# Kernel tuning notes

Hardware: AMD Instinct MI355X
Metric: run time of the kernel (lower is better)

The kernel has to match this reference:

```python
import jax, jax.numpy as jnp
import numpy as np

B, C, H, W = 2, 256, 32, 32
D_MODEL = C
D_INNER = 2 * D_MODEL          # 512
D_STATE = 16
DT_RANK = (D_MODEL + 15) // 16  # 16
D_CONV = 4
LN_EPS = 1e-5


def setup_inputs() -> dict:
    key = jax.random.key(0)
    ks = jax.random.split(key, 32)

    def nrm(k, shape, s=0.02):
        return (jax.random.normal(k, shape) * s).astype(jnp.float32)

    inp = {"x": jax.random.normal(ks[0], (B, C, H, W), dtype=jnp.float32)}
    # LayerNorm params
    inp["ln1_w"] = jnp.ones((D_MODEL,), jnp.float32)
    inp["ln1_b"] = jnp.zeros((D_MODEL,), jnp.float32)
    inp["ln2_w"] = jnp.ones((D_MODEL,), jnp.float32)
    inp["ln2_b"] = jnp.zeros((D_MODEL,), jnp.float32)
    # Two MambaBlocks with identical structure
    for i, p in enumerate(["m1", "m2"]):
        o = 1 + i * 11
        inp[p + "_in_w"] = nrm(ks[o + 0], (D_MODEL, 2 * D_INNER))
        inp[p + "_in_b"] = jnp.zeros((2 * D_INNER,), jnp.float32)
        inp[p + "_conv_w"] = nrm(ks[o + 1], (D_INNER, 1, D_CONV), 0.1)
        inp[p + "_conv_b"] = jnp.zeros((D_INNER,), jnp.float32)
        inp[p + "_xproj_w"] = nrm(ks[o + 2], (D_INNER, DT_RANK + 2 * D_STATE))
        inp[p + "_dt_w"] = nrm(ks[o + 3], (DT_RANK, D_INNER), 0.1)
        inp[p + "_dt_b"] = (jax.random.uniform(ks[o + 4], (D_INNER,)) * 0.1 - 4.0).astype(jnp.float32)
        # S4D-real init: A[d, n] = n+1
        inp[p + "_A_log"] = jnp.log(jnp.broadcast_to(jnp.arange(1, D_STATE + 1, dtype=jnp.float32), (D_INNER, D_STATE)))
        inp[p + "_D"] = jnp.ones((D_INNER,), jnp.float32)
        inp[p + "_out_w"] = nrm(ks[o + 5], (D_INNER, D_MODEL))
        inp[p + "_out_b"] = jnp.zeros((D_MODEL,), jnp.float32)
    return inp


def layernorm(x, w, b):
    mu = jnp.mean(x, axis=-1, keepdims=True)
    var = jnp.mean(jnp.square(x - mu), axis=-1, keepdims=True)
    return (x - mu) * jax.lax.rsqrt(var + LN_EPS) * w + b


def mamba_block(x, in_w, in_b, conv_w, conv_b, xproj_w, dt_w, dt_b, A_log, Dp, out_w, out_b):
    # x: (b, h, w, c) -> flatten spatial dims into the scan sequence
    b, h, w, c = x.shape
    L = h * w
    u = x.reshape(b, L, c)
    xr = u @ in_w + in_b                       # (b, L, 2*d_inner)
    xs, res = jnp.split(xr, 2, axis=-1)
    # depthwise causal conv1d over L
    xc = jnp.transpose(xs, (0, 2, 1))          # (b, d_inner, L)
    xc = jax.lax.conv_general_dilated(
        xc, conv_w, (1,), [(D_CONV - 1, 0)],
        dimension_numbers=("NCH", "OIH", "NCH"),
        feature_group_count=D_INNER) + conv_b[None, :, None]
    xs = jax.nn.silu(jnp.transpose(xc, (0, 2, 1)))  # (b, L, d_inner)
    # input-dependent SSM params
    x_dbl = xs @ xproj_w                       # (b, L, dt_rank + 2*n)
    dt, Bm, Cm = jnp.split(x_dbl, [DT_RANK, DT_RANK + D_STATE], axis=-1)
    delta = jax.nn.softplus(dt @ dt_w + dt_b)  # (b, L, d_inner)
    A = -jnp.exp(A_log)                        # (d_inner, n)
    dA = jnp.exp(delta[..., None] * A)                         # (b, L, d, n)
    dBu = delta[..., None] * Bm[:, :, None, :] * xs[..., None]  # (b, L, d, n)

    def step(hst, ins):
        dA_t, dBu_t, C_t = ins
        hst = dA_t * hst + dBu_t               # (b, d, n)
        y_t = jnp.einsum("bdn,bn->bd", hst, C_t)
        return hst, y_t

    h0 = jnp.zeros((b, D_INNER, D_STATE), dtype=xs.dtype)
    _, ys = jax.lax.scan(step, h0,
                         (jnp.swapaxes(dA, 0, 1), jnp.swapaxes(dBu, 0, 1), jnp.swapaxes(Cm, 0, 1)))
    y = jnp.swapaxes(ys, 0, 1) + xs * Dp       # (b, L, d_inner)
    y = y * jax.nn.silu(res)
    out = y @ out_w + out_b                    # (b, L, c)
    return out.reshape(b, h, w, c)


def reference(x, ln1_w, ln1_b, ln2_w, ln2_b,
              m1_in_w, m1_in_b, m1_conv_w, m1_conv_b, m1_xproj_w, m1_dt_w, m1_dt_b, m1_A_log, m1_D, m1_out_w, m1_out_b,
              m2_in_w, m2_in_b, m2_conv_w, m2_conv_b, m2_xproj_w, m2_dt_w, m2_dt_b, m2_A_log, m2_D, m2_out_w, m2_out_b):
    xt = jnp.transpose(x, (0, 2, 3, 1))  # b c h w -> b h w c
    xt = xt + layernorm(mamba_block(xt, m1_in_w, m1_in_b, m1_conv_w, m1_conv_b, m1_xproj_w,
                                    m1_dt_w, m1_dt_b, m1_A_log, m1_D, m1_out_w, m1_out_b), ln1_w, ln1_b)
    xt = jnp.flip(xt, axis=3)  # flip channel axis, as in the original
    xt = xt + layernorm(mamba_block(xt, m2_in_w, m2_in_b, m2_conv_w, m2_conv_b, m2_xproj_w,
                                    m2_dt_w, m2_dt_b, m2_A_log, m2_D, m2_out_w, m2_out_b), ln2_w, ln2_b)
    xt = jnp.flip(xt, axis=3)
    return jnp.transpose(xt, (0, 3, 1, 2))  # b h w c -> b c h w
```

## Files before the change

kernel.cpp:

```cpp
#include <hip/hip_runtime.h>
#include <hip/hip_bf16.h>
#include <math.h>

#define L 1024
#define NB 2
#define DM 256
#define DI 512
#define DS 16
#define DR 16
#define NC 64
#define CL 16

typedef unsigned int u32;
typedef short s16x8 __attribute__((ext_vector_type(8)));
typedef float f32x4 __attribute__((ext_vector_type(4)));

__device__ __forceinline__ float sigmoidf_(float x){ return 1.f/(1.f+__expf(-x)); }

__device__ __forceinline__ unsigned short f2bf(float v){
  u32 x = __float_as_uint(v);
  u32 r = (x + 0x7fffu + ((x >> 16) & 1u)) >> 16;
  return (unsigned short)r;
}

__device__ __forceinline__ void gload_lds16(const void* g, void* l){
  __builtin_amdgcn_global_load_lds((const __attribute__((address_space(1))) u32*)g,
                                   (__attribute__((address_space(3))) u32*)l, 16, 0, 0);
}

__device__ __forceinline__ void wave_reduce2(float& a, float& b){
  #pragma unroll
  for (int m=32; m; m>>=1){ a += __shfl_xor(a, m, 64); b += __shfl_xor(b, m, 64); }
}

#define SEG1 262144
#define SEG2 294912
#define SEG3 131072
#define SEGP (SEG1+SEG2+SEG3)
__global__ __launch_bounds__(256) void k_prep(
    const float* __restrict__ inw1, const float* __restrict__ xpw1, const float* __restrict__ dtw1, const float* __restrict__ outw1,
    const float* __restrict__ inw2, const float* __restrict__ xpw2, const float* __restrict__ dtw2, const float* __restrict__ outw2,
    unsigned short* __restrict__ Wt1i, unsigned short* __restrict__ Wt1x, unsigned short* __restrict__ Wt1o,
    unsigned short* __restrict__ Wt2i, unsigned short* __restrict__ Wt2x, unsigned short* __restrict__ Wt2o){
  int g = blockIdx.x*256 + threadIdx.x;
  int p = g >= SEGP;
  int r = g - p*SEGP;
  const float* inw = p ? inw2 : inw1;  const float* xpw = p ? xpw2 : xpw1;
  const float* dtw = p ? dtw2 : dtw1;  const float* outw = p ? outw2 : outw1;
  unsigned short* Wti = p ? Wt2i : Wt1i; unsigned short* Wtx = p ? Wt2x : Wt1x;
  unsigned short* Wto = p ? Wt2o : Wt1o;
  if (r < SEG1){
    int n = r >> 8, k = r & 255;
    Wti[r] = f2bf(inw[(size_t)k*1024 + n]);
  } else if (r < SEG1+SEG2){
    int q = r - SEG1; int n = q >> 9, k = q & 511;
    float v;
    if (n < 512){
      float acc = 0.f;
      #pragma unroll
      for (int j=0;j<16;++j) acc = fmaf(xpw[k*48 + j], dtw[j*512 + n], acc);
      v = acc;
    } else if (n < 544){
      v = xpw[k*48 + 16 + (n - 512)];
    } else v = 0.f;
    Wtx[q] = f2bf(v);
  } else {
    int q = r - SEG1 - SEG2; int n = q >> 9, k = q & 511;
    Wto[q] = f2bf(outw[(size_t)k*256 + n]);
  }
}

__global__ __launch_bounds__(256) void k_transpose_in(const float* __restrict__ x,
    float* __restrict__ u, unsigned short* __restrict__ ub){
  __shared__ float T[64][65];
  int t = threadIdx.x;
  int bidx = blockIdx.x;
  int lt = bidx & 15, ct = (bidx >> 4) & 3, b = bidx >> 6;
  int l0 = lt*64, c0 = ct*64;
  int lsub = (t & 15)*4, csub = t >> 4;
  #pragma unroll
  for (int i=0;i<4;++i){
    int c = csub + i*16;
    float4 v = *(const float4*)(x + ((size_t)(b*256 + c0 + c))*1024 + l0 + lsub);
    T[lsub+0][c]=v.x; T[lsub+1][c]=v.y; T[lsub+2][c]=v.z; T[lsub+3][c]=v.w;
  }
  __syncthreads();
  int cw = (t & 15)*4, lw = t >> 4;
  #pragma unroll
  for (int i=0;i<4;++i){
    int l = lw + i*16;
    float4 v = make_float4(T[l][cw], T[l][cw+1], T[l][cw+2], T[l][cw+3]);
    size_t o = ((size_t)(b*1024 + l0 + l))*256 + c0 + cw;
    *(float4*)(u + o) = v;
    *(ushort4*)(ub + o) = make_ushort4(f2bf(v.x), f2bf(v.y), f2bf(v.z), f2bf(v.w));
  }
}

__global__ __launch_bounds__(256) void k_gemm_mfma(const unsigned short* __restrict__ A,
    const unsigned short* __restrict__ Wt, const float* __restrict__ bias,
    float* __restrict__ C, int M, int N, int K){
  __shared__ __align__(16) unsigned short As[64*64];
  __shared__ __align__(16) unsigned short Bs[64*64];
  int tid = threadIdx.x;
  int lane = tid & 63;
  int wid  = tid >> 6;
  int bm = blockIdx.y * 64, bn = blockIdx.x * 64;
  int wm = (wid >> 1) * 32, wn = (wid & 1) * 32;
  int lrow = lane & 15, lg = lane >> 4;
  int srow = tid >> 3;
  int ssl  = tid & 7;
  int sswz = ssl ^ (srow & 7);

  f32x4 acc[2][2] = {};

  for (int k0 = 0; k0 < K; k0 += 64){
    #pragma unroll
    for (int i = 0; i < 2; ++i){
      int row = srow + i*32;
      gload_lds16(A  + (size_t)(bm + row)*K + k0 + sswz*8, &As[row*64 + ssl*8]);
      gload_lds16(Wt + (size_t)(bn + row)*K + k0 + sswz*8, &Bs[row*64 + ssl*8]);
    }
    __syncthreads();
    #pragma unroll
    for (int ks = 0; ks < 2; ++ks){
      int kg = ks*4 + lg;
      int swz = (kg ^ (lrow & 7)) << 3;
      s16x8 a[2], b[2];
      #pragma unroll
      for (int f = 0; f < 2; ++f){
        a[f] = *(const s16x8*)&As[(wm + f*16 + lrow)*64 + swz];
        b[f] = *(const s16x8*)&Bs[(wn + f*16 + lrow)*64 + swz];
      }
      #pragma unroll
      for (int i = 0; i < 2; ++i)
        #pragma unroll
        for (int j = 0; j < 2; ++j)
          acc[i][j] = __builtin_amdgcn_mfma_f32_16x16x32_bf16(a[i], b[j], acc[i][j], 0, 0, 0);
    }
    __syncthreads();
  }
  #pragma unroll
  for (int j = 0; j < 2; ++j){
    int col = bn + wn + j*16 + lrow;
    if (col < N){
      float bv = bias ? bias[col] : 0.f;
      #pragma unroll
      for (int i = 0; i < 2; ++i){
        #pragma unroll
        for (int r = 0; r < 4; ++r){
          int row = bm + wm + i*16 + lg*4 + r;
          C[(size_t)row*N + col] = acc[i][j][r] + bv;
        }
      }
    }
  }
}

__global__ __launch_bounds__(256) void k_gemm_xproj(const unsigned short* __restrict__ A,
    const unsigned short* __restrict__ Wt, const float* __restrict__ dtb,
    float* __restrict__ dlt, float* __restrict__ BC, int M){
  const int K = 512;
  __shared__ __align__(16) unsigned short As[64*64];
  __shared__ __align__(16) unsigned short Bs[64*64];
  int tid = threadIdx.x;
  int lane = tid & 63;
  int wid  = tid >> 6;
  int bm = blockIdx.y * 64, bn = blockIdx.x * 64;
  int wm = (wid >> 1) * 32, wn = (wid & 1) * 32;
  int lrow = lane & 15, lg = lane >> 4;
  int srow = tid >> 3;
  int ssl  = tid & 7;
  int sswz = ssl ^ (srow & 7);

  f32x4 acc[2][2] = {};

  for (int k0 = 0; k0 < K; k0 += 64){
    #pragma unroll
    for (int i = 0; i < 2; ++i){
      int row = srow + i*32;
      gload_lds16(A  + (size_t)(bm + row)*K + k0 + sswz*8, &As[row*64 + ssl*8]);
      gload_lds16(Wt + (size_t)(bn + row)*K + k0 + sswz*8, &Bs[row*64 + ssl*8]);
    }
    __syncthreads();
    #pragma unroll
    for (int ks = 0; ks < 2; ++ks){
      int kg = ks*4 + lg;
      int swz = (kg ^ (lrow & 7)) << 3;
      s16x8 a[2], b[2];
      #pragma unroll
      for (int f = 0; f < 2; ++f){
        a[f] = *(const s16x8*)&As[(wm + f*16 + lrow)*64 + swz];
        b[f] = *(const s16x8*)&Bs[(wn + f*16 + lrow)*64 + swz];
      }
      #pragma unroll
      for (int i = 0; i < 2; ++i)
        #pragma unroll
        for (int j = 0; j < 2; ++j)
          acc[i][j] = __builtin_amdgcn_mfma_f32_16x16x32_bf16(a[i], b[j], acc[i][j], 0, 0, 0);
    }
    __syncthreads();
  }
  #pragma unroll
  for (int j = 0; j < 2; ++j){
    int col = bn + wn + j*16 + lrow;
    if (col < 512){
      float bv = dtb[col];
      #pragma unroll
      for (int i = 0; i < 2; ++i){
        #pragma unroll
        for (int r = 0; r < 4; ++r){
          int row = bm + wm + i*16 + lg*4 + r;
          float a = acc[i][j][r] + bv;
          dlt[(size_t)row*512 + col] = fmaxf(a, 0.f) + log1pf(__expf(-fabsf(a)));
        }
      }
    } else if (col < 544){
      #pragma unroll
      for (int i = 0; i < 2; ++i){
        #pragma unroll
        for (int r = 0; r < 4; ++r){
          int row = bm + wm + i*16 + lg*4 + r;
          BC[(size_t)row*32 + (col - 512)] = acc[i][j][r];
        }
      }
    }
  }
}

__global__ __launch_bounds__(256) void k_conv_silu(const float* __restrict__ xr, const float* __restrict__ cw,
    const float* __restrict__ cb, float* __restrict__ xsc, unsigned short* __restrict__ xscb){
  int g = blockIdx.x*256 + threadIdx.x;
  int d = g & 511; int l = (g >> 9) & 1023; int b = g >> 19;
  float acc = cb[d];
  const float* w = cw + d*4;
  #pragma unroll
  for (int k=0;k<4;++k){
    int j = l + k - 3;
    if (j >= 0) acc = fmaf(w[k], xr[((size_t)(b*L + j))*(2*DI) + d], acc);
  }
  float v = acc * sigmoidf_(acc);
  xsc[g] = v; xscb[g] = f2bf(v);
}

__global__ __launch_bounds__(256) void k_scan_partial(const float* __restrict__ delta, const float* __restrict__ xsc,
    const float* __restrict__ BC, const float* __restrict__ A_log,
    float* __restrict__ hend, float* __restrict__ Ssum){
  int g = blockIdx.x*256 + threadIdx.x;
  int d = g & 511; int bc = g >> 9;
  int c = bc & (NC-1); int b = bc >> 6;
  float A[DS];
  #pragma unroll
  for (int n=0;n<DS;++n) A[n] = -__expf(A_log[d*DS + n]);
  float h[DS];
  #pragma unroll
  for (int n=0;n<DS;++n) h[n] = 0.f;
  float S = 0.f;
  int l0 = c*CL;
  for (int t=0;t<CL;++t){
    size_t ix = (size_t)(b*L + l0 + t);
    float dlt = delta[ix*DI + d];
    float xv  = xsc[ix*DI + d];
    S += dlt;
    float dx = dlt * xv;
    const float* bp = BC + ix*32;
    #pragma unroll
    for (int n=0;n<DS;++n){
      float dA = __expf(dlt * A[n]);
      h[n] = fmaf(dA, h[n], dx * bp[n]);
    }
  }
  #pragma unroll
  for (int n=0;n<DS;++n) hend[((size_t)bc*DS + n)*DI + d] = h[n];
  Ssum[(size_t)bc*DI + d] = S;
}

__global__ __launch_bounds__(256) void k_scan_combine(const float* __restrict__ hend, const float* __restrict__ Ssum,
    const float* __restrict__ A_log, float* __restrict__ hinit){
  int g = blockIdx.x*256 + threadIdx.x;
  int d = g & 511; int n = (g >> 9) & 15; int b = g >> 13;
  float A = -__expf(A_log[d*DS + n]);
  float h = 0.f;
  for (int c=0;c<NC;++c){
    int bc = b*NC + c;
    hinit[((size_t)bc*DS + n)*DI + d] = h;
    float dec = __expf(A * Ssum[(size_t)bc*DI + d]);
    h = fmaf(dec, h, hend[((size_t)bc*DS + n)*DI + d]);
  }
}

__global__ __launch_bounds__(256) void k_scan_final(const float* __restrict__ delta, const float* __restrict__ xsc,
    const float* __restrict__ BC, const float* __restrict__ xr, const float* __restrict__ A_log,
    const float* __restrict__ Dp, const float* __restrict__ hinit, unsigned short* __restrict__ ygb){
  int g = blockIdx.x*256 + threadIdx.x;
  int d = g & 511; int bc = g >> 9;
  int c = bc & (NC-1); int b = bc >> 6;
  float A[DS];
  #pragma unroll
  for (int n=0;n<DS;++n) A[n] = -__expf(A_log[d*DS + n]);
  float h[DS];
  #pragma unroll
  for (int n=0;n<DS;++n) h[n] = hinit[((size_t)bc*DS + n)*DI + d];
  float Dv = Dp[d];
  int l0 = c*CL;
  for (int t=0;t<CL;++t){
    size_t ix = (size_t)(b*L + l0 + t);
    float dlt = delta[ix*DI + d];
    float xv  = xsc[ix*DI + d];
    float res = xr[ix*(2*DI) + DI + d];
    float dx = dlt * xv;
    const float* bp = BC + ix*32;
    const float* cp = bp + 16;
    float y = 0.f;
    #pragma unroll
    for (int n=0;n<DS;++n){
      float dA = __expf(dlt * A[n]);
      h[n] = fmaf(dA, h[n], dx * bp[n]);
      y = fmaf(h[n], cp[n], y);
    }
    y = fmaf(xv, Dv, y);
    ygb[ix*DI + d] = f2bf(y * (res * sigmoidf_(res)));
  }
}

__global__ __launch_bounds__(256) void k_ln_flip(const float* __restrict__ mo, const float* __restrict__ resid,
    const float* __restrict__ w, const float* __restrict__ bias,
    float* __restrict__ u2, unsigned short* __restrict__ u2b){
  int row = blockIdx.x*4 + (threadIdx.x >> 6);
  int lane = threadIdx.x & 63;
  int c4 = lane*4;
  float4 xv = *(const float4*)(mo + (size_t)row*256 + c4);
  float s1 = xv.x+xv.y+xv.z+xv.w;
  float s2 = xv.x*xv.x+xv.y*xv.y+xv.z*xv.z+xv.w*xv.w;
  wave_reduce2(s1, s2);
  float mu = s1*(1.f/256), var = s2*(1.f/256) - mu*mu;
  float inv = rsqrtf(var + 1e-5f);
  float4 rv = *(const float4*)(resid + (size_t)row*256 + c4);
  float4 wv = *(const float4*)(w + c4);
  float4 bv = *(const float4*)(bias + c4);
  float o0 = rv.x + (xv.x-mu)*inv*wv.x + bv.x;
  float o1 = rv.y + (xv.y-mu)*inv*wv.y + bv.y;
  float o2 = rv.z + (xv.z-mu)*inv*wv.z + bv.z;
  float o3 = rv.w + (xv.w-mu)*inv*wv.w + bv.w;
  size_t o = (size_t)row*256 + (252 - c4);
  *(float4*)(u2 + o) = make_float4(o3, o2, o1, o0);
  *(ushort4*)(u2b + o) = make_ushort4(f2bf(o3), f2bf(o2), f2bf(o1), f2bf(o0));
}

__global__ __launch_bounds__(256) void k_ln_out(const float* __restrict__ mo, const float* __restrict__ resid,
    const float* __restrict__ w, const float* __restrict__ bias, float* __restrict__ out){
  int row = blockIdx.x*4 + (threadIdx.x >> 6);
  int lane = threadIdx.x & 63;
  int c4 = lane*4;
  int b = row >> 10, l = row & 1023;
  float4 xv = *(const float4*)(mo + (size_t)row*256 + c4);
  float s1 = xv.x+xv.y+xv.z+xv.w;
  float s2 = xv.x*xv.x+xv.y*xv.y+xv.z*xv.z+xv.w*xv.w;
  wave_reduce2(s1, s2);
  float mu = s1*(1.f/256), var = s2*(1.f/256) - mu*mu;
  float inv = rsqrtf(var + 1e-5f);
  float4 rv = *(const float4*)(resid + (size_t)row*256 + c4);
  float4 wv = *(const float4*)(w + c4);
  float4 bv = *(const float4*)(bias + c4);
  float o0 = rv.x + (xv.x-mu)*inv*wv.x + bv.x;
  float o1 = rv.y + (xv.y-mu)*inv*wv.y + bv.y;
  float o2 = rv.z + (xv.z-mu)*inv*wv.z + bv.z;
  float o3 = rv.w + (xv.w-mu)*inv*wv.w + bv.w;
  size_t base = ((size_t)b*256 + 255) << 10;
  out[base - ((size_t)(c4+0) << 10) + l] = o0;
  out[base - ((size_t)(c4+1) << 10) + l] = o1;
  out[base - ((size_t)(c4+2) << 10) + l] = o2;
  out[base - ((size_t)(c4+3) << 10) + l] = o3;
}

static void run_block(const unsigned short* ub, const float* inb, const float* cw, const float* cb,
                      const float* dtb, const float* Alog, const float* Dp, const float* ob,
                      const unsigned short* Wti, const unsigned short* Wtx, const unsigned short* Wto,
                      float* xr, float* xsc, unsigned short* xscb, float* dlt, float* BC,
                      unsigned short* ygb, float* hend, float* hinit, float* Ssum, float* mo,
                      hipStream_t stream){
  dim3 b256(256);
  k_gemm_mfma<<<dim3(16,32), b256, 0, stream>>>(ub, Wti, inb, xr, NB*L, 2*DI, DM);
  k_conv_silu<<<4096, b256, 0, stream>>>(xr, cw, cb, xsc, xscb);
  k_gemm_xproj<<<dim3(9,32), b256, 0, stream>>>(xscb, Wtx, dtb, dlt, BC, NB*L);
  k_scan_partial<<<NB*NC*DI/256, b256, 0, stream>>>(dlt, xsc, BC, Alog, hend, Ssum);
  k_scan_combine<<<NB*DS*DI/256, b256, 0, stream>>>(hend, Ssum, Alog, hinit);
  k_scan_final<<<NB*NC*DI/256, b256, 0, stream>>>(dlt, xsc, BC, xr, Alog, Dp, hinit, ygb);
  k_gemm_mfma<<<dim3(4,32), b256, 0, stream>>>(ygb, Wto, ob, mo, NB*L, DM, DI);
}

extern "C" void kernel_launch(void* const* d_in, const int* in_sizes, int n_in,
                              void* d_out, int out_size, void* d_ws, size_t ws_size,
                              hipStream_t stream) {
  const float* x    = (const float*)d_in[0];
  const float* ln1w = (const float*)d_in[1];
  const float* ln1b = (const float*)d_in[2];
  const float* ln2w = (const float*)d_in[3];
  const float* ln2b = (const float*)d_in[4];

  const float* m1[11]; const float* m2[11];
  for (int i=0;i<11;++i){ m1[i] = (const float*)d_in[5+i]; m2[i] = (const float*)d_in[16+i]; }

  float* ws = (float*)d_ws;
  float*          u0   = ws;
  unsigned short* u0b  = (unsigned short*)(ws + 524288);
  float*          xr   = ws + 655360;
  float*          xsc  = ws + 2752512;
  unsigned short* xscb = (unsigned short*)(ws + 3801088);
  float*          dlt  = ws + 4063232;
  float*          BC   = ws + 5111808;
  unsigned short* ygb  = (unsigned short*)(ws + 5177344);
  float*          hend = ws + 5439488;
  float*          hinit= ws + 6488064;
  float*          Ssum = ws + 7536640;
  float*          u2   = ws + 7602176;
  unsigned short* Wt1i = (unsigned short*)(ws + 8126464);
  unsigned short* Wt1x = (unsigned short*)(ws + 8257536);
  unsigned short* Wt1o = (unsigned short*)(ws + 8404992);
  unsigned short* Wt2i = (unsigned short*)(ws + 8470528);
  unsigned short* Wt2x = (unsigned short*)(ws + 8601600);
  unsigned short* Wt2o = (unsigned short*)(ws + 8749056);
  unsigned short* u2b = u0b;
  float* mo = hend;

  dim3 b256(256);
  k_prep<<<2*SEGP/256, b256, 0, stream>>>(m1[0], m1[4], m1[5], m1[9],
                                          m2[0], m2[4], m2[5], m2[9],
                                          Wt1i, Wt1x, Wt1o, Wt2i, Wt2x, Wt2o);
  k_transpose_in<<<128, b256, 0, stream>>>(x, u0, u0b);

  run_block(u0b, m1[1], m1[2], m1[3], m1[6], m1[7], m1[8], m1[10],
            Wt1i, Wt1x, Wt1o, xr, xsc, xscb, dlt, BC, ygb, hend, hinit, Ssum, mo, stream);
  k_ln_flip<<<512, b256, 0, stream>>>(mo, u0, ln1w, ln1b, u2, u2b);

  run_block(u2b, m2[1], m2[2], m2[3], m2[6], m2[7], m2[8], m2[10],
            Wt2i, Wt2x, Wt2o, xr, xsc, xscb, dlt, BC, ygb, hend, hinit, Ssum, mo, stream);
  k_ln_out<<<512, b256, 0, stream>>>(mo, u2, ln2w, ln2b, (float*)d_out);
}
```

Baseline: 155.6 us.

## Fuse scan stages, out-proj GEMM with LayerNorm, and prep with transpose

Merges the three scan kernels into one block-local kernel that keeps chunk end-states in LDS, which removes the hend/hinit global round trips and two launches. Fuses the output projection GEMM with the residual LayerNorm and flip, using a full-row 64x256 tile so row statistics can be reduced in-block. Also merges the weight prep with the input transpose, and vectorises the conv+silu to four channels per thread. The cost is less parallelism: the scan now runs only 256 blocks, the combine step is serial over 64 chunks on one wave, and the out-LN GEMM launches just 32 blocks.

```diff
diff --git a/kernel.cpp b/kernel.cpp
--- a/kernel.cpp
+++ b/kernel.cpp
@@ -28,21 +28,42 @@
                                    (__attribute__((address_space(3))) u32*)l, 16, 0, 0);
 }
 
-__device__ __forceinline__ void wave_reduce2(float& a, float& b){
-  #pragma unroll
-  for (int m=32; m; m>>=1){ a += __shfl_xor(a, m, 64); b += __shfl_xor(b, m, 64); }
-}
-
 #define SEG1 262144
 #define SEG2 294912
 #define SEG3 131072
 #define SEGP (SEG1+SEG2+SEG3)
-__global__ __launch_bounds__(256) void k_prep(
+__global__ __launch_bounds__(256) void k_prep_trans(const float* __restrict__ x,
+    float* __restrict__ u, unsigned short* __restrict__ ub,
     const float* __restrict__ inw1, const float* __restrict__ xpw1, const float* __restrict__ dtw1, const float* __restrict__ outw1,
     const float* __restrict__ inw2, const float* __restrict__ xpw2, const float* __restrict__ dtw2, const float* __restrict__ outw2,
     unsigned short* __restrict__ Wt1i, unsigned short* __restrict__ Wt1x, unsigned short* __restrict__ Wt1o,
     unsigned short* __restrict__ Wt2i, unsigned short* __restrict__ Wt2x, unsigned short* __restrict__ Wt2o){
-  int g = blockIdx.x*256 + threadIdx.x;
+  __shared__ float T[64][65];
+  if (blockIdx.x < 128){
+    int t = threadIdx.x;
+    int bidx = blockIdx.x;
+    int lt = bidx & 15, ct = (bidx >> 4) & 3, b = bidx >> 6;
+    int l0 = lt*64, c0 = ct*64;
+    int lsub = (t & 15)*4, csub = t >> 4;
+    #pragma unroll
+    for (int i=0;i<4;++i){
+      int c = csub + i*16;
+      float4 v = *(const float4*)(x + ((size_t)(b*256 + c0 + c))*1024 + l0 + lsub);
+      T[lsub+0][c]=v.x; T[lsub+1][c]=v.y; T[lsub+2][c]=v.z; T[lsub+3][c]=v.w;
+    }
+    __syncthreads();
+    int cw = (t & 15)*4, lw = t >> 4;
+    #pragma unroll
+    for (int i=0;i<4;++i){
+      int l = lw + i*16;
+      float4 v = make_float4(T[l][cw], T[l][cw+1], T[l][cw+2], T[l][cw+3]);
+      size_t o = ((size_t)(b*1024 + l0 + l))*256 + c0 + cw;
+      *(float4*)(u + o) = v;
+      *(ushort4*)(ub + o) = make_ushort4(f2bf(v.x), f2bf(v.y), f2bf(v.z), f2bf(v.w));
+    }
+    return;
+  }
+  int g = (blockIdx.x - 128)*256 + threadIdx.x;
   int p = g >= SEGP;
   int r = g - p*SEGP;
   const float* inw = p ? inw2 : inw1;  const float* xpw = p ? xpw2 : xpw1;
@@ -67,32 +88,6 @@
   } else {
     int q = r - SEG1 - SEG2; int n = q >> 9, k = q & 511;
     Wto[q] = f2bf(outw[(size_t)k*256 + n]);
-  }
-}
-
-__global__ __launch_bounds__(256) void k_transpose_in(const float* __restrict__ x,
-    float* __restrict__ u, unsigned short* __restrict__ ub){
-  __shared__ float T[64][65];
-  int t = threadIdx.x;
-  int bidx = blockIdx.x;
-  int lt = bidx & 15, ct = (bidx >> 4) & 3, b = bidx >> 6;
-  int l0 = lt*64, c0 = ct*64;
-  int lsub = (t & 15)*4, csub = t >> 4;
-  #pragma unroll
-  for (int i=0;i<4;++i){
-    int c = csub + i*16;
-    float4 v = *(const float4*)(x + ((size_t)(b*256 + c0 + c))*1024 + l0 + lsub);
-    T[lsub+0][c]=v.x; T[lsub+1][c]=v.y; T[lsub+2][c]=v.z; T[lsub+3][c]=v.w;
-  }
-  __syncthreads();
-  int cw = (t & 15)*4, lw = t >> 4;
-  #pragma unroll
-  for (int i=0;i<4;++i){
-    int l = lw + i*16;
-    float4 v = make_float4(T[l][cw], T[l][cw+1], T[l][cw+2], T[l][cw+3]);
-    size_t o = ((size_t)(b*1024 + l0 + l))*256 + c0 + cw;
-    *(float4*)(u + o) = v;
-    *(ushort4*)(ub + o) = make_ushort4(f2bf(v.x), f2bf(v.y), f2bf(v.z), f2bf(v.w));
   }
 }
 
@@ -227,27 +222,44 @@
   }
 }
 
-__global__ __launch_bounds__(256) void k_conv_silu(const float* __restrict__ xr, const float* __restrict__ cw,
+__global__ __launch_bounds__(256) void k_conv4(const float* __restrict__ xr, const float* __restrict__ cw,
     const float* __restrict__ cb, float* __restrict__ xsc, unsigned short* __restrict__ xscb){
   int g = blockIdx.x*256 + threadIdx.x;
-  int d = g & 511; int l = (g >> 9) & 1023; int b = g >> 19;
-  float acc = cb[d];
-  const float* w = cw + d*4;
+  int i4 = g << 2;
+  int d = i4 & 511; int l = (i4 >> 9) & 1023; int b = i4 >> 19;
+  float4 w0 = *(const float4*)(cw + (d+0)*4);
+  float4 w1 = *(const float4*)(cw + (d+1)*4);
+  float4 w2 = *(const float4*)(cw + (d+2)*4);
+  float4 w3 = *(const float4*)(cw + (d+3)*4);
+  float4 a = *(const float4*)(cb + d);
+  const float* p0 = (const float*)&w0; const float* p1 = (const float*)&w1;
+  const float* p2 = (const float*)&w2; const float* p3 = (const float*)&w3;
   #pragma unroll
   for (int k=0;k<4;++k){
     int j = l + k - 3;
-    if (j >= 0) acc = fmaf(w[k], xr[((size_t)(b*L + j))*(2*DI) + d], acc);
-  }
-  float v = acc * sigmoidf_(acc);
-  xsc[g] = v; xscb[g] = f2bf(v);
-}
-
-__global__ __launch_bounds__(256) void k_scan_partial(const float* __restrict__ delta, const float* __restrict__ xsc,
-    const float* __restrict__ BC, const float* __restrict__ A_log,
-    float* __restrict__ hend, float* __restrict__ Ssum){
-  int g = blockIdx.x*256 + threadIdx.x;
-  int d = g & 511; int bc = g >> 9;
-  int c = bc & (NC-1); int b = bc >> 6;
+    if (j >= 0){
+      float4 xv = *(const float4*)(xr + ((size_t)(b*L + j))*(2*DI) + d);
+      a.x = fmaf(p0[k], xv.x, a.x);
+      a.y = fmaf(p1[k], xv.y, a.y);
+      a.z = fmaf(p2[k], xv.z, a.z);
+      a.w = fmaf(p3[k], xv.w, a.w);
+    }
+  }
+  a.x *= sigmoidf_(a.x); a.y *= sigmoidf_(a.y);
+  a.z *= sigmoidf_(a.z); a.w *= sigmoidf_(a.w);
+  *(float4*)(xsc + i4) = a;
+  *(ushort4*)(xscb + i4) = make_ushort4(f2bf(a.x), f2bf(a.y), f2bf(a.z), f2bf(a.w));
+}
+
+__global__ __launch_bounds__(256) void k_scan_fused(const float* __restrict__ delta,
+    const float* __restrict__ xsc, const float* __restrict__ BC, const float* __restrict__ xr,
+    const float* __restrict__ A_log, const float* __restrict__ Dp, unsigned short* __restrict__ ygb){
+  __shared__ float hbuf[64][68];
+  __shared__ float SsumL[64][4];
+  int tid = threadIdx.x;
+  int chunk = tid >> 2, dl = tid & 3;
+  int b = blockIdx.x >> 7, d0 = (blockIdx.x & 127) << 2;
+  int d = d0 + dl;
   float A[DS];
   #pragma unroll
   for (int n=0;n<DS;++n) A[n] = -__expf(A_log[d*DS + n]);
@@ -255,7 +267,7 @@
   #pragma unroll
   for (int n=0;n<DS;++n) h[n] = 0.f;
   float S = 0.f;
-  int l0 = c*CL;
+  int l0 = chunk*CL;
   for (int t=0;t<CL;++t){
     size_t ix = (size_t)(b*L + l0 + t);
     float dlt = delta[ix*DI + d];
@@ -264,44 +276,28 @@
     float dx = dlt * xv;
     const float* bp = BC + ix*32;
     #pragma unroll
-    for (int n=0;n<DS;++n){
-      float dA = __expf(dlt * A[n]);
-      h[n] = fmaf(dA, h[n], dx * bp[n]);
-    }
-  }
-  #pragma unroll
-  for (int n=0;n<DS;++n) hend[((size_t)bc*DS + n)*DI + d] = h[n];
-  Ssum[(size_t)bc*DI + d] = S;
-}
-
-__global__ __launch_bounds__(256) void k_scan_combine(const float* __restrict__ hend, const float* __restrict__ Ssum,
-    const float* __restrict__ A_log, float* __restrict__ hinit){
-  int g = blockIdx.x*256 + threadIdx.x;
-  int d = g & 511; int n = (g >> 9) & 15; int b = g >> 13;
-  float A = -__expf(A_log[d*DS + n]);
-  float h = 0.f;
-  for (int c=0;c<NC;++c){
-    int bc = b*NC + c;
-    hinit[((size_t)bc*DS + n)*DI + d] = h;
-    float dec = __expf(A * Ssum[(size_t)bc*DI + d]);
-    h = fmaf(dec, h, hend[((size_t)bc*DS + n)*DI + d]);
-  }
-}
-
-__global__ __launch_bounds__(256) void k_scan_final(const float* __restrict__ delta, const float* __restrict__ xsc,
-    const float* __restrict__ BC, const float* __restrict__ xr, const float* __restrict__ A_log,
-    const float* __restrict__ Dp, const float* __restrict__ hinit, unsigned short* __restrict__ ygb){
-  int g = blockIdx.x*256 + threadIdx.x;
-  int d = g & 511; int bc = g >> 9;
-  int c = bc & (NC-1); int b = bc >> 6;
-  float A[DS];
-  #pragma unroll
-  for (int n=0;n<DS;++n) A[n] = -__expf(A_log[d*DS + n]);
-  float h[DS];
-  #pragma unroll
-  for (int n=0;n<DS;++n) h[n] = hinit[((size_t)bc*DS + n)*DI + d];
+    for (int n=0;n<DS;++n) h[n] = fmaf(__expf(dlt*A[n]), h[n], dx * bp[n]);
+  }
+  #pragma unroll
+  for (int n=0;n<DS;++n) hbuf[chunk][dl*16+n] = h[n];
+  SsumL[chunk][dl] = S;
+  __syncthreads();
+  if (tid < 64){
+    int dl2 = tid & 3, n2 = tid >> 2;
+    float An = -__expf(A_log[(d0+dl2)*DS + n2]);
+    float hh = 0.f;
+    for (int c=0;c<NC;++c){
+      float he  = hbuf[c][dl2*16+n2];
+      float dec = __expf(An * SsumL[c][dl2]);
+      float nh  = fmaf(dec, hh, he);
+      hbuf[c][dl2*16+n2] = hh;
+      hh = nh;
+    }
+  }
+  __syncthreads();
+  #pragma unroll
+  for (int n=0;n<DS;++n) h[n] = hbuf[chunk][dl*16+n];
   float Dv = Dp[d];
-  int l0 = c*CL;
   for (int t=0;t<CL;++t){
     size_t ix = (size_t)(b*L + l0 + t);
     float dlt = delta[ix*DI + d];
@@ -313,8 +309,7 @@
     float y = 0.f;
     #pragma unroll
     for (int n=0;n<DS;++n){
-      float dA = __expf(dlt * A[n]);
-      h[n] = fmaf(dA, h[n], dx * bp[n]);
+      h[n] = fmaf(__expf(dlt*A[n]), h[n], dx * bp[n]);
       y = fmaf(h[n], cp[n], y);
     }
     y = fmaf(xv, Dv, y);
@@ -322,70 +317,93 @@
   }
 }
 
-__global__ __launch_bounds__(256) void k_ln_flip(const float* __restrict__ mo, const float* __restrict__ resid,
-    const float* __restrict__ w, const float* __restrict__ bias,
-    float* __restrict__ u2, unsigned short* __restrict__ u2b){
-  int row = blockIdx.x*4 + (threadIdx.x >> 6);
-  int lane = threadIdx.x & 63;
-  int c4 = lane*4;
-  float4 xv = *(const float4*)(mo + (size_t)row*256 + c4);
-  float s1 = xv.x+xv.y+xv.z+xv.w;
-  float s2 = xv.x*xv.x+xv.y*xv.y+xv.z*xv.z+xv.w*xv.w;
-  wave_reduce2(s1, s2);
-  float mu = s1*(1.f/256), var = s2*(1.f/256) - mu*mu;
-  float inv = rsqrtf(var + 1e-5f);
-  float4 rv = *(const float4*)(resid + (size_t)row*256 + c4);
-  float4 wv = *(const float4*)(w + c4);
-  float4 bv = *(const float4*)(bias + c4);
-  float o0 = rv.x + (xv.x-mu)*inv*wv.x + bv.x;
-  float o1 = rv.y + (xv.y-mu)*inv*wv.y + bv.y;
-  float o2 = rv.z + (xv.z-mu)*inv*wv.z + bv.z;
-  float o3 = rv.w + (xv.w-mu)*inv*wv.w + bv.w;
-  size_t o = (size_t)row*256 + (252 - c4);
-  *(float4*)(u2 + o) = make_float4(o3, o2, o1, o0);
-  *(ushort4*)(u2b + o) = make_ushort4(f2bf(o3), f2bf(o2), f2bf(o1), f2bf(o0));
-}
-
-__global__ __launch_bounds__(256) void k_ln_out(const float* __restrict__ mo, const float* __restrict__ resid,
-    const float* __restrict__ w, const float* __restrict__ bias, float* __restrict__ out){
-  int row = blockIdx.x*4 + (threadIdx.x >> 6);
-  int lane = threadIdx.x & 63;
-  int c4 = lane*4;
-  int b = row >> 10, l = row & 1023;
-  float4 xv = *(const float4*)(mo + (size_t)row*256 + c4);
-  float s1 = xv.x+xv.y+xv.z+xv.w;
-  float s2 = xv.x*xv.x+xv.y*xv.y+xv.z*xv.z+xv.w*xv.w;
-  wave_reduce2(s1, s2);
-  float mu = s1*(1.f/256), var = s2*(1.f/256) - mu*mu;
-  float inv = rsqrtf(var + 1e-5f);
-  float4 rv = *(const float4*)(resid + (size_t)row*256 + c4);
-  float4 wv = *(const float4*)(w + c4);
-  float4 bv = *(const float4*)(bias + c4);
-  float o0 = rv.x + (xv.x-mu)*inv*wv.x + bv.x;
-  float o1 = rv.y + (xv.y-mu)*inv*wv.y + bv.y;
-  float o2 = rv.z + (xv.z-mu)*inv*wv.z + bv.z;
-  float o3 = rv.w + (xv.w-mu)*inv*wv.w + bv.w;
-  size_t base = ((size_t)b*256 + 255) << 10;
-  out[base - ((size_t)(c4+0) << 10) + l] = o0;
-  out[base - ((size_t)(c4+1) << 10) + l] = o1;
-  out[base - ((size_t)(c4+2) << 10) + l] = o2;
-  out[base - ((size_t)(c4+3) << 10) + l] = o3;
-}
-
-static void run_block(const unsigned short* ub, const float* inb, const float* cw, const float* cb,
-                      const float* dtb, const float* Alog, const float* Dp, const float* ob,
-                      const unsigned short* Wti, const unsigned short* Wtx, const unsigned short* Wto,
-                      float* xr, float* xsc, unsigned short* xscb, float* dlt, float* BC,
-                      unsigned short* ygb, float* hend, float* hinit, float* Ssum, float* mo,
-                      hipStream_t stream){
-  dim3 b256(256);
-  k_gemm_mfma<<<dim3(16,32), b256, 0, stream>>>(ub, Wti, inb, xr, NB*L, 2*DI, DM);
-  k_conv_silu<<<4096, b256, 0, stream>>>(xr, cw, cb, xsc, xscb);
-  k_gemm_xproj<<<dim3(9,32), b256, 0, stream>>>(xscb, Wtx, dtb, dlt, BC, NB*L);
-  k_scan_partial<<<NB*NC*DI/256, b256, 0, stream>>>(dlt, xsc, BC, Alog, hend, Ssum);
-  k_scan_combine<<<NB*DS*DI/256, b256, 0, stream>>>(hend, Ssum, Alog, hinit);
-  k_scan_final<<<NB*NC*DI/256, b256, 0, stream>>>(dlt, xsc, BC, xr, Alog, Dp, hinit, ygb);
-  k_gemm_mfma<<<dim3(4,32), b256, 0, stream>>>(ygb, Wto, ob, mo, NB*L, DM, DI);
+template<int MODE>
+__global__ __launch_bounds__(256) void k_gemm_out_ln(const unsigned short* __restrict__ A,
+    const unsigned short* __restrict__ Wt, const float* __restrict__ ob,
+    const float* __restrict__ resid, const float* __restrict__ lnw, const float* __restrict__ lnb,
+    float* __restrict__ out, unsigned short* __restrict__ outb){
+  __shared__ __align__(16) unsigned short As[64*64];
+  __shared__ __align__(16) unsigned short Bs[256*64];
+  __shared__ float redS[2][64], redQ[2][64];
+  int tid = threadIdx.x, lane = tid & 63, wid = tid >> 6;
+  int bm = blockIdx.x * 64;
+  int wm = (wid & 1)*32, wn = (wid >> 1)*128;
+  int lrow = lane & 15, lg = lane >> 4;
+  int srow = tid >> 3, ssl = tid & 7;
+  int sswz = ssl ^ (srow & 7);
+  f32x4 acc[2][8] = {};
+  for (int k0=0;k0<512;k0+=64){
+    #pragma unroll
+    for (int i=0;i<2;++i){
+      int row = srow + i*32;
+      gload_lds16(A + (size_t)(bm+row)*512 + k0 + sswz*8, &As[row*64 + ssl*8]);
+    }
+    #pragma unroll
+    for (int i=0;i<8;++i){
+      int row = srow + i*32;
+      gload_lds16(Wt + (size_t)row*512 + k0 + sswz*8, &Bs[row*64 + ssl*8]);
+    }
+    __syncthreads();
+    #pragma unroll
+    for (int ks=0;ks<2;++ks){
+      int kg = ks*4 + lg;
+      int swz = (kg ^ (lrow & 7)) << 3;
+      s16x8 a[2], bq[8];
+      #pragma unroll
+      for (int f=0;f<2;++f) a[f] = *(const s16x8*)&As[(wm + f*16 + lrow)*64 + swz];
+      #pragma unroll
+      for (int j=0;j<8;++j) bq[j] = *(const s16x8*)&Bs[(wn + j*16 + lrow)*64 + swz];
+      #pragma unroll
+      for (int f=0;f<2;++f)
+        #pragma unroll
+        for (int j=0;j<8;++j)
+          acc[f][j] = __builtin_amdgcn_mfma_f32_16x16x32_bf16(a[f], bq[j], acc[f][j], 0, 0, 0);
+    }
+    __syncthreads();
+  }
+  float bv[8], lw[8], lb[8];
+  #pragma unroll
+  for (int j=0;j<8;++j){
+    int col = wn + j*16 + lrow;
+    bv[j] = ob[col]; lw[j] = lnw[col]; lb[j] = lnb[col];
+  }
+  #pragma unroll
+  for (int i=0;i<2;++i)
+    #pragma unroll
+    for (int r=0;r<4;++r){
+      float s=0.f, q=0.f;
+      #pragma unroll
+      for (int j=0;j<8;++j){ float v = acc[i][j][r] + bv[j]; s += v; q = fmaf(v, v, q); }
+      #pragma unroll
+      for (int m=1;m<=8;m<<=1){ s += __shfl_xor(s, m, 64); q += __shfl_xor(q, m, 64); }
+      if (lrow == 0){ int row = wm + i*16 + lg*4 + r; redS[wn>>7][row] = s; redQ[wn>>7][row] = q; }
+    }
+  __syncthreads();
+  #pragma unroll
+  for (int i=0;i<2;++i)
+    #pragma unroll
+    for (int r=0;r<4;++r){
+      int row = wm + i*16 + lg*4 + r;
+      int grow = bm + row;
+      float S = redS[0][row] + redS[1][row];
+      float Q = redQ[0][row] + redQ[1][row];
+      float mu = S * (1.f/256.f);
+      float var = Q * (1.f/256.f) - mu*mu;
+      float inv = rsqrtf(var + 1e-5f);
+      #pragma unroll
+      for (int j=0;j<8;++j){
+        int col = wn + j*16 + lrow;
+        float v = acc[i][j][r] + bv[j];
+        float o = resid[(size_t)grow*256 + col] + (v - mu)*inv*lw[j] + lb[j];
+        if (MODE == 0){
+          out[(size_t)grow*256 + 255 - col]  = o;
+          outb[(size_t)grow*256 + 255 - col] = f2bf(o);
+        } else {
+          int bb = grow >> 10, ll = grow & 1023;
+          out[(((size_t)bb*256) + (255 - col))*1024 + ll] = o;
+        }
+      }
+    }
 }
 
 extern "C" void kernel_launch(void* const* d_in, const int* in_sizes, int n_in,
@@ -406,33 +424,32 @@
   float*          xr   = ws + 655360;
   float*          xsc  = ws + 2752512;
   unsigned short* xscb = (unsigned short*)(ws + 3801088);
-  float*          dlt  = ws + 4063232;
-  float*          BC   = ws + 5111808;
-  unsigned short* ygb  = (unsigned short*)(ws + 5177344);
-  float*          hend = ws + 5439488;
-  float*          hinit= ws + 6488064;
-  float*          Ssum = ws + 7536640;
-  float*          u2   = ws + 7602176;
-  unsigned short* Wt1i = (unsigned short*)(ws + 8126464);
-  unsigned short* Wt1x = (unsigned short*)(ws + 8257536);
-  unsigned short* Wt1o = (unsigned short*)(ws + 8404992);
-  unsigned short* Wt2i = (unsigned short*)(ws + 8470528);
-  unsigned short* Wt2x = (unsigned short*)(ws + 8601600);
-  unsigned short* Wt2o = (unsigned short*)(ws + 8749056);
-  unsigned short* u2b = u0b;
-  float* mo = hend;
+  float*          dlt  = ws + 4325376;
+  float*          BC   = ws + 5373952;
+  unsigned short* ygb  = (unsigned short*)(ws + 5439488);
+  float*          u2   = ws + 5963776;
+  unsigned short* u2b  = (unsigned short*)(ws + 6488064);
+  unsigned short* Wt1i = (unsigned short*)(ws + 6619136);
+  unsigned short* Wt1x = (unsigned short*)(ws + 6750208);
+  unsigned short* Wt1o = (unsigned short*)(ws + 6897664);
+  unsigned short* Wt2i = (unsigned short*)(ws + 6963200);
+  unsigned short* Wt2x = (unsigned short*)(ws + 7094272);
+  unsigned short* Wt2o = (unsigned short*)(ws + 7241728);
 
   dim3 b256(256);
-  k_prep<<<2*SEGP/256, b256, 0, stream>>>(m1[0], m1[4], m1[5], m1[9],
-                                          m2[0], m2[4], m2[5], m2[9],
-                                          Wt1i, Wt1x, Wt1o, Wt2i, Wt2x, Wt2o);
-  k_transpose_in<<<128, b256, 0, stream>>>(x, u0, u0b);
-
-  run_block(u0b, m1[1], m1[2], m1[3], m1[6], m1[7], m1[8], m1[10],
-            Wt1i, Wt1x, Wt1o, xr, xsc, xscb, dlt, BC, ygb, hend, hinit, Ssum, mo, stream);
-  k_ln_flip<<<512, b256, 0, stream>>>(mo, u0, ln1w, ln1b, u2, u2b);
-
-  run_block(u2b, m2[1], m2[2], m2[3], m2[6], m2[7], m2[8], m2[10],
-            Wt2i, Wt2x, Wt2o, xr, xsc, xscb, dlt, BC, ygb, hend, hinit, Ssum, mo, stream);
-  k_ln_out<<<512, b256, 0, stream>>>(mo, u2, ln2w, ln2b, (float*)d_out);
-}
+  k_prep_trans<<<128 + 2*SEGP/256, b256, 0, stream>>>(x, u0, u0b,
+      m1[0], m1[4], m1[5], m1[9], m2[0], m2[4], m2[5], m2[9],
+      Wt1i, Wt1x, Wt1o, Wt2i, Wt2x, Wt2o);
+
+  k_gemm_mfma<<<dim3(16,32), b256, 0, stream>>>(u0b, Wt1i, m1[1], xr, NB*L, 2*DI, DM);
+  k_conv4<<<1024, b256, 0, stream>>>(xr, m1[2], m1[3], xsc, xscb);
+  k_gemm_xproj<<<dim3(9,32), b256, 0, stream>>>(xscb, Wt1x, m1[6], dlt, BC, NB*L);
+  k_scan_fused<<<NB*DI/4, b256, 0, stream>>>(dlt, xsc, BC, xr, m1[7], m1[8], ygb);
+  k_gemm_out_ln<0><<<32, b256, 0, stream>>>(ygb, Wt1o, m1[10], u0, ln1w, ln1b, u2, u2b);
+
+  k_gemm_mfma<<<dim3(16,32), b256, 0, stream>>>(u2b, Wt2i, m2[1], xr, NB*L, 2*DI, DM);
+  k_conv4<<<1024, b256, 0, stream>>>(xr, m2[2], m2[3], xsc, xscb);
+  k_gemm_xproj<<<dim3(9,32), b256, 0, stream>>>(xscb, Wt2x, m2[6], dlt, BC, NB*L);
+  k_scan_fused<<<NB*DI/4, b256, 0, stream>>>(dlt, xsc, BC, xr, m2[7], m2[8], ygb);
+  k_gemm_out_ln<1><<<32, b256, 0, stream>>>(ygb, Wt2o, m2[10], u2, ln2w, ln2b, (float*)d_out, nullptr);
+}
```

Result: slower. 164.0 us (+5.4%).
